# Kernel optimization log

Hardware: AMD Instinct MI355X
Metric: run time of the kernel (lower is better)

## Reference

```python
import jax, jax.numpy as jnp
import numpy as np

MODES = 2
LC = 4
N = 6000
KNN = 10
NODES = 64
CH = MODES ** 2
M = N * 2 * (KNN + 1)  # total candidate couplings


def setup_inputs() -> dict:
    key = jax.random.key(0)
    ks = jax.random.split(key, 6)
    return {
        "CK_inputs": jax.random.normal(ks[0], (N, 2 * (KNN + 1), 3), dtype=jnp.float32),
        "W_in": jax.random.normal(ks[1], (3, NODES), dtype=jnp.float32) * 0.1,
        "b_in": jnp.zeros((NODES,), dtype=jnp.float32),
        "W_hid": jax.random.normal(ks[2], (LC - 1, NODES, NODES), dtype=jnp.float32) * 0.1,
        "b_hid": jnp.zeros((LC - 1, NODES), dtype=jnp.float32),
        "W_out": jax.random.normal(ks[3], (NODES, CH), dtype=jnp.float32) * 0.1,
        "b_out": jnp.zeros((CH,), dtype=jnp.float32),
        "coo": jax.random.randint(ks[4], (2, M), 0, N, dtype=jnp.int32),
    }


def _mlp(x, W_in, b_in, W_hid, b_hid, W_out, b_out):
    # MLP: 3 -> 64, (LC-1) hidden 64->64 layers, 64 -> CH; ReLU activations.
    h = jax.nn.relu(x @ W_in + b_in)
    for i in range(W_hid.shape[0]):  # small fixed layer count
        h = jax.nn.relu(h @ W_hid[i] + b_hid[i])
    return h @ W_out + b_out  # [M, CH]


def reference(CK_inputs, W_in, b_in, W_hid, b_hid, W_out, b_out, coo):
    C_stripped = _mlp(CK_inputs.reshape(-1, 3), W_in, b_in, W_hid, b_hid, W_out, b_out)  # [M, CH]
    D = MODES * N
    # Original: for channel ch = mi*MODES+mj, scatter C_stripped[:, ch] at indices coo*MODES+mj
    # (mj added to BOTH row and col, replicating the source exactly). Indices are
    # independent of mi, so sum over mi first, then one scatter-add per mj.
    vals = C_stripped.reshape(-1, MODES, MODES).sum(axis=1)  # [M, MODES]; axis1=mi, axis2=mj
    dense = jnp.zeros((D, D), dtype=CK_inputs.dtype)
    for mj in range(MODES):
        idx = coo * MODES + mj  # [2, M]
        dense = dense.at[idx[0], idx[1]].add(vals[:, mj])
    return dense
```

## Files before the change

### kernel.cpp

```cpp
#include <hip/hip_runtime.h>
#include <stdint.h>

#define NN    6000
#define KNNC  10
#define MM    (NN * 2 * (KNNC + 1))
#define DD    (2 * NN)
#define LCH   3
#define BLK   256

#define RB     128
#define RPL    2
#define MLPGRID ((MM + RB - 1) / RB)
#define SCGRID  ((MM + BLK - 1) / BLK)
#define OUTBYTES ((size_t)DD * DD * 4)

#define MAXB     128
#define VALS_B   (MM * 2 * 4)
#define CNT_B    (NN * 4)
#define BINS_B   (NN * MAXB * 4)
#define WS_NEEDED (VALS_B + CNT_B + BINS_B)


__global__ void zero_cnt(int* __restrict__ cnt) {
    const int i = blockIdx.x * BLK + threadIdx.x;
    if (i < NN) cnt[i] = 0;
}

__global__ __launch_bounds__(BLK, 4) void mlp_bin(
    const float* __restrict__ CK,
    const float* __restrict__ Win,
    const float* __restrict__ bin,
    const float* __restrict__ Whid,
    const float* __restrict__ bhid,
    const float* __restrict__ Wout,
    const float* __restrict__ bout,
    const int* __restrict__ coo,
    float* __restrict__ vals,
    int* __restrict__ cnt,
    int* __restrict__ bins,
    const int do_bins)
{
    __shared__ float sH[64 * RB];

    const int tid  = threadIdx.x;
    const int wave = tid >> 6;
    const int lane = tid & 63;
    const int jo = __builtin_amdgcn_readfirstlane((tid >> 6) << 4);

    const int rbase = blockIdx.x * RB;
    const int mb0   = rbase + lane * 2;
    const int mb    = mb0 < MM ? mb0 : MM - 2;

    const float2 ca = *(const float2*)(CK + mb * 3);
    const float2 cb = *(const float2*)(CK + mb * 3 + 2);
    const float2 cc = *(const float2*)(CK + mb * 3 + 4);
    const float x0[RPL] = {ca.x, cb.y};
    const float x1[RPL] = {ca.y, cc.x};
    const float x2[RPL] = {cb.x, cc.y};

#pragma unroll
    for (int jj = 0; jj < 16; jj++) {
        const int j = jo + jj;
        const float w0 = Win[j], w1 = Win[64 + j], w2 = Win[128 + j];
        const float bj = bin[j];
        float2 hv;
        hv.x = fmaxf(fmaf(x2[0], w2, fmaf(x1[0], w1, fmaf(x0[0], w0, bj))), 0.f);
        hv.y = fmaxf(fmaf(x2[1], w2, fmaf(x1[1], w1, fmaf(x0[1], w0, bj))), 0.f);
        *(float2*)(sH + j * RB + lane * 2) = hv;
    }
    __syncthreads();

#pragma unroll 1
    for (int l = 0; l < LCH; l++) {
        const float* __restrict__ Wl = Whid + (l << 12) + jo;
        const float* __restrict__ bh = bhid + (l << 6) + jo;

        float g[RPL][16];
#pragma unroll
        for (int jj = 0; jj < 16; jj++) {
            const float bj = bh[jj];
            g[0][jj] = bj;
            g[1][jj] = bj;
        }

#pragma unroll 4
        for (int k = 0; k < 64; k++) {
            const float4 wa = *(const float4*)(Wl + (k << 6));
            const float4 wb = *(const float4*)(Wl + (k << 6) + 4);
            const float4 wc = *(const float4*)(Wl + (k << 6) + 8);
            const float4 wd = *(const float4*)(Wl + (k << 6) + 12);
            const float2 hv = *(const float2*)(sH + k * RB + lane * 2);
            const float hk[RPL] = {hv.x, hv.y};
#pragma unroll
            for (int r = 0; r < RPL; r++) {
                g[r][0]  = fmaf(wa.x, hk[r], g[r][0]);
                g[r][1]  = fmaf(wa.y, hk[r], g[r][1]);
                g[r][2]  = fmaf(wa.z, hk[r], g[r][2]);
                g[r][3]  = fmaf(wa.w, hk[r], g[r][3]);
                g[r][4]  = fmaf(wb.x, hk[r], g[r][4]);
                g[r][5]  = fmaf(wb.y, hk[r], g[r][5]);
                g[r][6]  = fmaf(wb.z, hk[r], g[r][6]);
                g[r][7]  = fmaf(wb.w, hk[r], g[r][7]);
                g[r][8]  = fmaf(wc.x, hk[r], g[r][8]);
                g[r][9]  = fmaf(wc.y, hk[r], g[r][9]);
                g[r][10] = fmaf(wc.z, hk[r], g[r][10]);
                g[r][11] = fmaf(wc.w, hk[r], g[r][11]);
                g[r][12] = fmaf(wd.x, hk[r], g[r][12]);
                g[r][13] = fmaf(wd.y, hk[r], g[r][13]);
                g[r][14] = fmaf(wd.z, hk[r], g[r][14]);
                g[r][15] = fmaf(wd.w, hk[r], g[r][15]);
            }
        }
        __syncthreads();

#pragma unroll
        for (int jj = 0; jj < 16; jj++) {
            float2 hv;
            hv.x = fmaxf(g[0][jj], 0.f);
            hv.y = fmaxf(g[1][jj], 0.f);
            *(float2*)(sH + (jo + jj) * RB + lane * 2) = hv;
        }
        __syncthreads();
    }

    float v0[RPL], v1[RPL];
    const float b02 = bout[0] + bout[2], b13 = bout[1] + bout[3];
#pragma unroll
    for (int r = 0; r < RPL; r++) { v0[r] = b02; v1[r] = b13; }
#pragma unroll 8
    for (int k = 0; k < 64; k++) {
        const float4 wo = ((const float4*)Wout)[k];
        const float wxz = wo.x + wo.z, wyw = wo.y + wo.w;
        const float2 hv = *(const float2*)(sH + k * RB + lane * 2);
        v0[0] = fmaf(hv.x, wxz, v0[0]);  v1[0] = fmaf(hv.x, wyw, v1[0]);
        v0[1] = fmaf(hv.y, wxz, v0[1]);  v1[1] = fmaf(hv.y, wyw, v1[1]);
    }
    if (wave == 0 && mb0 < MM) {
        *(float4*)(vals + 2 * mb0) = make_float4(v0[0], v1[0], v0[1], v1[1]);
        if (do_bins) {
#pragma unroll
            for (int r = 0; r < RPL; r++) {
                const int m = mb0 + r;
                const int i = coo[m];
                const int pos = atomicAdd(&cnt[i], 1);
                if (pos < MAXB) bins[i * MAXB + pos] = m;
            }
        }
    }
}

__global__ __launch_bounds__(BLK) void fill_patch(
    const float* __restrict__ vals,
    const int* __restrict__ coo,
    const int* __restrict__ cnt,
    const int* __restrict__ bins,
    float* __restrict__ out)
{
    const int bid = blockIdx.x;
    const int i   = bid >> 1;
    const int mj  = bid & 1;
    const int tid = threadIdx.x;

    float* __restrict__ rowp = out + (size_t)(2 * i + mj) * DD;

    const float4 z = make_float4(0.f, 0.f, 0.f, 0.f);
    for (int j = tid; j < DD / 4; j += BLK) ((float4*)rowp)[j] = z;

    __syncthreads();

    int n = cnt[i];
    n = n < 0 ? 0 : (n > MAXB ? MAXB : n);
    for (int e = tid; e < n; e += BLK) {
        const int m = bins[i * MAXB + e];
        const int c = coo[MM + m] * 2 + mj;
        unsafeAtomicAdd(rowp + c, vals[2 * m + mj]);
    }
}

__global__ __launch_bounds__(BLK) void scatter_add(
    const float* __restrict__ vals, const int* __restrict__ coo,
    float* __restrict__ out)
{
    const int t = blockIdx.x * BLK + threadIdx.x;
    if (t >= MM) return;
    const int r2 = coo[t] * 2;
    const int c2 = coo[MM + t] * 2;
    const float2 v = *(const float2*)(vals + 2 * t);
    const long long f0 = (long long)r2 * DD + c2;
    unsafeAtomicAdd(out + f0, v.x);
    unsafeAtomicAdd(out + f0 + DD + 1, v.y);
}

extern "C" void kernel_launch(void* const* d_in, const int* in_sizes, int n_in,
                              void* d_out, int out_size, void* d_ws, size_t ws_size,
                              hipStream_t stream) {
    const float* CK   = (const float*)d_in[0];
    const float* Win  = (const float*)d_in[1];
    const float* bin  = (const float*)d_in[2];
    const float* Whid = (const float*)d_in[3];
    const float* bhid = (const float*)d_in[4];
    const float* Wout = (const float*)d_in[5];
    const float* bout = (const float*)d_in[6];
    const int* coo    = (const int*)d_in[7];
    float* out        = (float*)d_out;
    float* vals       = (float*)d_ws;

    if (ws_size >= (size_t)WS_NEEDED) {
        int* cnt  = (int*)((char*)d_ws + VALS_B);
        int* bins = (int*)((char*)d_ws + VALS_B + CNT_B);
        zero_cnt<<<(NN + BLK - 1) / BLK, BLK, 0, stream>>>(cnt);
        mlp_bin<<<MLPGRID, BLK, 0, stream>>>(
            CK, Win, bin, Whid, bhid, Wout, bout, coo, vals, cnt, bins, 1);
        fill_patch<<<2 * NN, BLK, 0, stream>>>(vals, coo, cnt, bins, out);
    } else {
        hipMemsetAsync(out, 0, OUTBYTES, stream);
        mlp_bin<<<MLPGRID, BLK, 0, stream>>>(
            CK, Win, bin, Whid, bhid, Wout, bout, coo, vals, nullptr, nullptr, 0);
        scatter_add<<<SCGRID, BLK, 0, stream>>>(vals, coo, out);
    }
}
```

Before: 665.2 us.

## Zero output via memset and patch rows with deduplicated plain stores

Replaces the per-row block that zeroed each output row and then applied atomic adds with a bulk device memset followed by a sparse patch kernel. The patch kernel assigns one wavefront per source node, stages column indices and values in shared memory, sums duplicate columns with a quadratic scan, and writes each unique entry once with a plain store. This aims to use the runtime's fill path for the dense zeroing and to remove atomic traffic, at the cost of an extra launch and quadratic per-row work.

```diff
diff --git a/kernel.cpp b/kernel.cpp
--- a/kernel.cpp
+++ b/kernel.cpp
@@ -15,11 +15,11 @@
 #define OUTBYTES ((size_t)DD * DD * 4)
 
 #define MAXB     128
+#define PROWS    4
 #define VALS_B   (MM * 2 * 4)
 #define CNT_B    (NN * 4)
 #define BINS_B   (NN * MAXB * 4)
 #define WS_NEEDED (VALS_B + CNT_B + BINS_B)
-
 
 __global__ void zero_cnt(int* __restrict__ cnt) {
     const int i = blockIdx.x * BLK + threadIdx.x;
@@ -149,31 +149,50 @@
     }
 }
 
-__global__ __launch_bounds__(BLK) void fill_patch(
+__global__ __launch_bounds__(BLK) void patch_rows(
     const float* __restrict__ vals,
     const int* __restrict__ coo,
     const int* __restrict__ cnt,
     const int* __restrict__ bins,
     float* __restrict__ out)
 {
-    const int bid = blockIdx.x;
-    const int i   = bid >> 1;
-    const int mj  = bid & 1;
-    const int tid = threadIdx.x;
-
-    float* __restrict__ rowp = out + (size_t)(2 * i + mj) * DD;
-
-    const float4 z = make_float4(0.f, 0.f, 0.f, 0.f);
-    for (int j = tid; j < DD / 4; j += BLK) ((float4*)rowp)[j] = z;
-
-    __syncthreads();
+    __shared__ int   cols[PROWS][MAXB];
+    __shared__ float sv0[PROWS][MAXB];
+    __shared__ float sv1[PROWS][MAXB];
+
+    const int tid  = threadIdx.x;
+    const int w    = tid >> 6;
+    const int lane = tid & 63;
+    const int i    = blockIdx.x * PROWS + w;
+    if (i >= NN) return;
 
     int n = cnt[i];
     n = n < 0 ? 0 : (n > MAXB ? MAXB : n);
-    for (int e = tid; e < n; e += BLK) {
+
+    for (int e = lane; e < n; e += 64) {
         const int m = bins[i * MAXB + e];
-        const int c = coo[MM + m] * 2 + mj;
-        unsafeAtomicAdd(rowp + c, vals[2 * m + mj]);
+        cols[w][e] = coo[MM + m];
+        const float2 v = *(const float2*)(vals + 2 * m);
+        sv0[w][e] = v.x;
+        sv1[w][e] = v.y;
+    }
+    __syncthreads();
+
+    for (int e = lane; e < n; e += 64) {
+        const int c = cols[w][e];
+        int first = -1;
+        float t0 = 0.f, t1 = 0.f;
+        for (int j = 0; j < n; j++) {
+            if (cols[w][j] == c) {
+                if (first < 0) first = j;
+                t0 += sv0[w][j];
+                t1 += sv1[w][j];
+            }
+        }
+        if (first == e) {
+            out[(size_t)(2 * i) * DD + 2 * c]           = t0;
+            out[(size_t)(2 * i + 1) * DD + 2 * c + 1]   = t1;
+        }
     }
 }
 
@@ -211,7 +230,9 @@
         zero_cnt<<<(NN + BLK - 1) / BLK, BLK, 0, stream>>>(cnt);
         mlp_bin<<<MLPGRID, BLK, 0, stream>>>(
             CK, Win, bin, Whid, bhid, Wout, bout, coo, vals, cnt, bins, 1);
-        fill_patch<<<2 * NN, BLK, 0, stream>>>(vals, coo, cnt, bins, out);
+        hipMemsetAsync(out, 0, OUTBYTES, stream);
+        patch_rows<<<(NN + PROWS - 1) / PROWS, BLK, 0, stream>>>(
+            vals, coo, cnt, bins, out);
     } else {
         hipMemsetAsync(out, 0, OUTBYTES, stream);
         mlp_bin<<<MLPGRID, BLK, 0, stream>>>(
```

After: 660.8 us. No clear change (-0.7%).

## Merge zero-fill and bin scatter into single-pass row writer with bitmap

Applied to the files above, without the earlier changes.

Replaces the per-(row,mj) zero-then-atomic-add fill with one block per node that stages its binned entries in shared memory and builds a bitmap of touched float4 columns. Each output float4 is written exactly once with its summed values, so there is no separate zeroing pass, no global atomics and no read-modify-write on the output. Both output rows of a node are now handled by one block. In exchange, a thread whose float4 is marked in the bitmap scans all n entries linearly.

```diff
diff --git a/kernel.cpp b/kernel.cpp
--- a/kernel.cpp
+++ b/kernel.cpp
@@ -15,6 +15,8 @@
 #define OUTBYTES ((size_t)DD * DD * 4)
 
 #define MAXB     128
+#define NF4      (DD / 4)
+#define NBW      96
 #define VALS_B   (MM * 2 * 4)
 #define CNT_B    (NN * 4)
 #define BINS_B   (NN * MAXB * 4)
@@ -149,31 +151,56 @@
     }
 }
 
-__global__ __launch_bounds__(BLK) void fill_patch(
+__global__ __launch_bounds__(BLK) void fill_merge(
     const float* __restrict__ vals,
     const int* __restrict__ coo,
     const int* __restrict__ cnt,
     const int* __restrict__ bins,
     float* __restrict__ out)
 {
-    const int bid = blockIdx.x;
-    const int i   = bid >> 1;
-    const int mj  = bid & 1;
+    __shared__ unsigned bmap[NBW];
+    __shared__ int   scol[MAXB];
+    __shared__ float sv0[MAXB];
+    __shared__ float sv1[MAXB];
+
+    const int i   = blockIdx.x;
     const int tid = threadIdx.x;
-
-    float* __restrict__ rowp = out + (size_t)(2 * i + mj) * DD;
-
-    const float4 z = make_float4(0.f, 0.f, 0.f, 0.f);
-    for (int j = tid; j < DD / 4; j += BLK) ((float4*)rowp)[j] = z;
-
-    __syncthreads();
 
     int n = cnt[i];
     n = n < 0 ? 0 : (n > MAXB ? MAXB : n);
-    for (int e = tid; e < n; e += BLK) {
-        const int m = bins[i * MAXB + e];
-        const int c = coo[MM + m] * 2 + mj;
-        unsafeAtomicAdd(rowp + c, vals[2 * m + mj]);
+
+    if (tid < NBW) bmap[tid] = 0u;
+    __syncthreads();
+
+    if (tid < n) {
+        const int m = bins[i * MAXB + tid];
+        const int c = coo[MM + m];
+        scol[tid] = c;
+        const float2 v = *(const float2*)(vals + 2 * m);
+        sv0[tid] = v.x;
+        sv1[tid] = v.y;
+        const int s = c >> 1;
+        atomicOr(&bmap[s >> 5], 1u << (s & 31));
+    }
+    __syncthreads();
+
+    float4* __restrict__ r0 = (float4*)(out + (size_t)(2 * i) * DD);
+    float4* __restrict__ r1 = (float4*)(out + (size_t)(2 * i + 1) * DD);
+
+    for (int f = tid; f < NF4; f += BLK) {
+        float4 a = make_float4(0.f, 0.f, 0.f, 0.f);
+        float4 b = make_float4(0.f, 0.f, 0.f, 0.f);
+        if (bmap[f >> 5] & (1u << (f & 31))) {
+            for (int e = 0; e < n; e++) {
+                const int c = scol[e];
+                if ((c >> 1) == f) {
+                    if ((c & 1) == 0) { a.x += sv0[e]; b.y += sv1[e]; }
+                    else              { a.z += sv0[e]; b.w += sv1[e]; }
+                }
+            }
+        }
+        r0[f] = a;
+        r1[f] = b;
     }
 }
 
@@ -211,7 +238,7 @@
         zero_cnt<<<(NN + BLK - 1) / BLK, BLK, 0, stream>>>(cnt);
         mlp_bin<<<MLPGRID, BLK, 0, stream>>>(
             CK, Win, bin, Whid, bhid, Wout, bout, coo, vals, cnt, bins, 1);
-        fill_patch<<<2 * NN, BLK, 0, stream>>>(vals, coo, cnt, bins, out);
+        fill_merge<<<NN, BLK, 0, stream>>>(vals, coo, cnt, bins, out);
     } else {
         hipMemsetAsync(out, 0, OUTBYTES, stream);
         mlp_bin<<<MLPGRID, BLK, 0, stream>>>(
```

Measured after the change: 652.1 us. 1.02x faster.
